# Performance work log

Hardware: AMD Instinct MI355X
Metric: run time of the kernel (lower is better)

The kernel has to match this reference:

```python
import jax, jax.numpy as jnp
import numpy as np

EPS = 1e-6  # torch nn.PairwiseDistance default eps


def setup_inputs() -> dict:
    key = jax.random.key(0)
    k1, k2 = jax.random.split(key)
    B, D, H, W = 4096, 512, 128, 128
    x = jax.random.normal(k1, (B, D), dtype=jnp.float32)
    weight = jax.random.normal(k2, (D, H * W), dtype=jnp.float32)  # SOM codebook (D, K)
    xs, ys = jnp.meshgrid(jnp.arange(H), jnp.arange(W), indexing="ij")
    locations = jnp.stack([xs.ravel(), ys.ravel()], axis=-1).astype(jnp.float32)  # (K, 2)
    return {"x": x, "weight": weight, "locations": locations}


def reference(x, weight, locations):
    # Faithful to torch: dists[b,k] = ||x[b,:] - weight[:,k] + eps||_2 reduced over D,
    # then min over codes, gather BMU grid locations, mean min-distance loss.
    B, D = x.shape
    x2 = jnp.sum(x * x, axis=1, keepdims=True)            # (B,1)
    w2 = jnp.sum(weight * weight, axis=0, keepdims=True)  # (1,K)
    cross = x @ weight                                     # (B,K) GEMM
    # exact expansion of sum_d (x - w + eps)^2
    lin = 2.0 * EPS * (jnp.sum(x, axis=1, keepdims=True) - jnp.sum(weight, axis=0, keepdims=True))
    d2 = x2 - 2.0 * cross + w2 + lin + jnp.float32(D) * EPS * EPS  # (B,K)
    dists = jnp.sqrt(jnp.maximum(d2, 0.0))
    losses = jnp.min(dists, axis=1, keepdims=True)         # (B,1)
    bmu_idx = jnp.argmin(dists, axis=1)                    # (B,)
    bmu_locations = locations[bmu_idx][:, None, :]         # (B,1,2) like locations[bmu_indexes]
    loss = jnp.sum(losses) / jnp.float32(B)
    return bmu_locations, loss
```

## Files before the change

### kernel.cpp

```cpp
#include <hip/hip_runtime.h>
#include <stdint.h>

#define B_ROWS 4096
#define D_DIM  512
#define K_CODES 16384
#define EPS 1e-6f

typedef __attribute__((ext_vector_type(8))) short short8;
typedef __attribute__((ext_vector_type(4))) float floatx4;

__device__ __forceinline__ unsigned short f2bf(float f) {
  unsigned int u = __float_as_uint(f);
  u += 0x7FFFu + ((u >> 16) & 1u);
  return (unsigned short)(u >> 16);
}
__device__ __forceinline__ float bf2f(unsigned short h) {
  return __uint_as_float(((unsigned int)h) << 16);
}

__device__ __forceinline__ void load_lds16(const short* g, short* l) {
  __builtin_amdgcn_global_load_lds(
      (const __attribute__((address_space(1))) void*)g,
      (__attribute__((address_space(3))) void*)l, 16, 0, 0);
}

__global__ void prep_kernel(const float* __restrict__ x,
                            const float* __restrict__ w,
                            short* __restrict__ A, short* __restrict__ W,
                            float* __restrict__ row_term,
                            float* __restrict__ colpart,
                            float* __restrict__ loss_acc,
                            unsigned int* __restrict__ counter) {
  const int bid = blockIdx.x;
  const int t = threadIdx.x;
  if (bid < 2048) {
    __shared__ float tile[64][65];
    const int k0 = (bid & 255) * 64;
    const int dchunk = bid >> 8;
    const int d0 = dchunk * 64;
#pragma unroll
    for (int i = 0; i < 4; ++i) {
      int idx = i * 256 + t;
      int r = idx >> 4, c4 = (idx & 15) * 4;
      float4 v = *(const float4*)&w[(size_t)(d0 + r) * K_CODES + k0 + c4];
      tile[r][c4 + 0] = v.x;
      tile[r][c4 + 1] = v.y;
      tile[r][c4 + 2] = v.z;
      tile[r][c4 + 3] = v.w;
    }
    __syncthreads();
    const int sub = t & 7;
    const int cd8 = sub * 8;
#pragma unroll
    for (int g = 0; g < 2; ++g) {
      const int rk = (t >> 3) + g * 32;
      short8 hi, lo;
      float s = 0.f, q = 0.f;
#pragma unroll
      for (int j = 0; j < 8; ++j) {
        float v = tile[cd8 + j][rk];
        s += v;
        q += v * v;
        unsigned short h = f2bf(v);
        float r2 = v - bf2f(h);
        hi[j] = (short)h;
        lo[j] = (short)f2bf(r2);
      }
      *(short8*)(W + (size_t)(k0 + rk) * 1024 + d0 + cd8) = hi;
      *(short8*)(W + (size_t)(k0 + rk) * 1024 + 512 + d0 + cd8) = lo;
#pragma unroll
      for (int m = 1; m < 8; m <<= 1) {
        s += __shfl_xor(s, m, 64);
        q += __shfl_xor(q, m, 64);
      }
      if (sub == 0)
        colpart[(size_t)dchunk * K_CODES + k0 + rk] = q - 2.0f * EPS * s;
    }
  } else {
    const int xb = bid - 2048;
    if (xb == 0 && t == 0) { loss_acc[0] = 0.0f; counter[0] = 0u; }
    const int wv = t >> 6, lane = t & 63;
#pragma unroll
    for (int i = 0; i < 4; ++i) {
      const int b = xb * 16 + i * 4 + wv;
      const float* xr = x + (size_t)b * D_DIM;
      float4 v0 = ((const float4*)xr)[lane * 2];
      float4 v1 = ((const float4*)xr)[lane * 2 + 1];
      float vals[8] = {v0.x, v0.y, v0.z, v0.w, v1.x, v1.y, v1.z, v1.w};
      short8 hi, lo;
      float s = 0.f, q = 0.f;
#pragma unroll
      for (int j = 0; j < 8; ++j) {
        float v = vals[j];
        s += v;
        q += v * v;
        unsigned short h = f2bf(v);
        float r = v - bf2f(h);
        hi[j] = (short)h;
        lo[j] = (short)f2bf(r);
      }
      *(short8*)(A + (size_t)b * 1024 + lane * 8) = hi;
      *(short8*)(A + (size_t)b * 1024 + 512 + lane * 8) = lo;
#pragma unroll
      for (int m = 1; m < 64; m <<= 1) {
        s += __shfl_xor(s, m, 64);
        q += __shfl_xor(q, m, 64);
      }
      if (lane == 0) row_term[b] = q + 2.0f * EPS * s + (float)D_DIM * EPS * EPS;
    }
  }
}

__global__ __launch_bounds__(256, 4) void som_gemm_kernel(
    const short* __restrict__ A, const short* __restrict__ W,
    const float* __restrict__ row_term, const float* __restrict__ colpart,
    unsigned long long* __restrict__ partial) {
  __shared__ __align__(16) short As[128 * 64];
  __shared__ __align__(16) short Bs[128 * 64];

  const int nt = blockIdx.x;
  const int mt = blockIdx.y;
  const int m0 = mt * 128, n0 = nt * 128;
  const int tid = threadIdx.x;
  const int wv = tid >> 6, lane = tid & 63;
  const int m_off = (wv & 1) * 64, n_off = (wv >> 1) * 64;
  const int q = lane >> 4, l15 = lane & 15;

  floatx4 acc[4][4];
  const floatx4 zero = {0.f, 0.f, 0.f, 0.f};
#pragma unroll
  for (int mi = 0; mi < 4; ++mi)
#pragma unroll
    for (int ni = 0; ni < 4; ++ni) acc[mi][ni] = zero;

  const int srow = lane >> 3;
  const int scol = ((lane & 7) ^ (srow & 7)) * 8;

  for (int kt = 0; kt < 24; ++kt) {
    const int a_k0 = (kt * 64) & 1023;
    const int w_k0 = (kt < 16) ? ((kt * 64) & 511) : (kt * 64 - 512);
    __syncthreads();
#pragma unroll
    for (int i = 0; i < 4; ++i) {
      const int c = wv * 4 + i;
      const int row = c * 8 + srow;
      load_lds16(A + (size_t)(m0 + row) * 1024 + a_k0 + scol, As + c * 512);
      load_lds16(W + (size_t)(n0 + row) * 1024 + w_k0 + scol, Bs + c * 512);
    }
    __syncthreads();
#pragma unroll
    for (int ks = 0; ks < 2; ++ks) {
      const int sw = ((ks * 4 + q) ^ (l15 & 7)) * 8;
      short8 af[4], bf[4];
#pragma unroll
      for (int mi = 0; mi < 4; ++mi)
        af[mi] = *(const short8*)(As + (m_off + mi * 16 + l15) * 64 + sw);
#pragma unroll
      for (int ni = 0; ni < 4; ++ni)
        bf[ni] = *(const short8*)(Bs + (n_off + ni * 16 + l15) * 64 + sw);
#pragma unroll
      for (int mi = 0; mi < 4; ++mi)
#pragma unroll
        for (int ni = 0; ni < 4; ++ni)
          acc[mi][ni] = __builtin_amdgcn_mfma_f32_16x16x32_bf16(
              af[mi], bf[ni], acc[mi][ni], 0, 0, 0);
    }
  }

  float ct[4];
#pragma unroll
  for (int ni = 0; ni < 4; ++ni) {
    const int k = n0 + n_off + ni * 16 + l15;
    float s = 0.f;
#pragma unroll
    for (int c = 0; c < 8; ++c) s += colpart[(size_t)c * K_CODES + k];
    ct[ni] = s;
  }
  float rt[16];
#pragma unroll
  for (int mi = 0; mi < 4; ++mi)
#pragma unroll
    for (int r = 0; r < 4; ++r)
      rt[mi * 4 + r] = row_term[m0 + m_off + mi * 16 + q * 4 + r];

  __syncthreads();
  unsigned long long* lds_min = (unsigned long long*)As;

#pragma unroll
  for (int mi = 0; mi < 4; ++mi) {
#pragma unroll
    for (int r = 0; r < 4; ++r) {
      unsigned long long v = ~0ull;
#pragma unroll
      for (int ni = 0; ni < 4; ++ni) {
        float d2 = rt[mi * 4 + r] + ct[ni] - 2.0f * acc[mi][ni][r];
        d2 = fmaxf(d2, 0.0f);
        unsigned long long p =
            ((unsigned long long)__float_as_uint(d2) << 32) |
            (unsigned int)(n0 + n_off + ni * 16 + l15);
        v = p < v ? p : v;
      }
#pragma unroll
      for (int mms = 1; mms < 16; mms <<= 1) {
        unsigned long long o = __shfl_xor(v, mms, 64);
        v = o < v ? o : v;
      }
      if (l15 == 0) lds_min[(wv >> 1) * 128 + m_off + mi * 16 + q * 4 + r] = v;
    }
  }
  __syncthreads();
  if (tid < 128) {
    unsigned long long v0 = lds_min[tid];
    unsigned long long v1 = lds_min[128 + tid];
    partial[(size_t)nt * B_ROWS + m0 + tid] = v1 < v0 ? v1 : v0;
  }
}

__global__ void finalize_kernel(const unsigned long long* __restrict__ partial,
                                const float* __restrict__ loc,
                                float* __restrict__ out,
                                float* __restrict__ loss_acc,
                                unsigned int* __restrict__ counter) {
  __shared__ unsigned long long red[4][64];
  const int t = threadIdx.x;
  const int rl = t & 63;
  const int p = t >> 6;
  const int b = blockIdx.x * 64 + rl;
  unsigned long long v = ~0ull;
#pragma unroll
  for (int i = 0; i < 32; ++i) {
    int nt = p * 32 + i;
    unsigned long long pv = partial[(size_t)nt * B_ROWS + b];
    v = pv < v ? pv : v;
  }
  red[p][rl] = v;
  __syncthreads();
  if (t < 64) {
    unsigned long long v0 = red[0][t], v1 = red[1][t];
    unsigned long long v2 = red[2][t], v3 = red[3][t];
    v0 = v1 < v0 ? v1 : v0;
    v2 = v3 < v2 ? v3 : v2;
    v0 = v2 < v0 ? v2 : v0;
    unsigned int k = (unsigned int)(v0 & 0xFFFFFFFFu);
    float d2 = __uint_as_float((unsigned int)(v0 >> 32));
    float dist = sqrtf(d2);
    int row = blockIdx.x * 64 + t;
    out[2 * row] = loc[2 * k];
    out[2 * row + 1] = loc[2 * k + 1];
    float s = dist;
#pragma unroll
    for (int m = 1; m < 64; m <<= 1) s += __shfl_xor(s, m, 64);
    if (t == 0) {
      atomicAdd(loss_acc, s);
      __threadfence();
      unsigned int old = atomicAdd(counter, 1u);
      if (old == gridDim.x - 1) {
        __threadfence();
        float total = atomicAdd(loss_acc, 0.0f);
        out[2 * B_ROWS] = total * (1.0f / (float)B_ROWS);
      }
    }
  }
}

extern "C" void kernel_launch(void* const* d_in, const int* in_sizes, int n_in,
                              void* d_out, int out_size, void* d_ws, size_t ws_size,
                              hipStream_t stream) {
  const float* x = (const float*)d_in[0];
  const float* w = (const float*)d_in[1];
  const float* loc = (const float*)d_in[2];
  float* out = (float*)d_out;
  char* ws = (char*)d_ws;

  short* A = (short*)(ws + 0);
  short* W = (short*)(ws + 8388608);
  float* row_term = (float*)(ws + 41943040);
  float* colpart = (float*)(ws + 41959424);
  unsigned long long* partial = (unsigned long long*)(ws + 42483712);
  float* loss_acc = (float*)(ws + 46678016);
  unsigned int* counter = (unsigned int*)(ws + 46678020);

  prep_kernel<<<2304, 256, 0, stream>>>(x, w, A, W, row_term, colpart,
                                        loss_acc, counter);
  som_gemm_kernel<<<dim3(K_CODES / 128, B_ROWS / 128), 256, 0, stream>>>(
      A, W, row_term, colpart, partial);
  finalize_kernel<<<B_ROWS / 64, 256, 0, stream>>>(partial, loc, out, loss_acc,
                                                   counter);
}
```

Baseline: 288.9 us.

## Add dedicated producer wave with double-buffered LDS to overlap loads and MFMA

The GEMM block grows to five waves. The extra wave does all global-to-LDS loads for the next K-tile into a second LDS buffer while the four compute waves run MFMAs on the current buffer. This removes one barrier per K step and aims to hide global load latency behind compute. In exchange, LDS per block doubles and the launch bounds drop to two blocks per CU. A single wave now has to issue every load, which could make load issue the bottleneck.

```diff
diff --git a/kernel.cpp b/kernel.cpp
--- a/kernel.cpp
+++ b/kernel.cpp
@@ -111,12 +111,12 @@
   }
 }
 
-__global__ __launch_bounds__(256, 4) void som_gemm_kernel(
+__global__ __launch_bounds__(320, 2) void som_gemm_kernel(
     const short* __restrict__ A, const short* __restrict__ W,
     const float* __restrict__ row_term, const float* __restrict__ colpart,
     unsigned long long* __restrict__ partial) {
-  __shared__ __align__(16) short As[128 * 64];
-  __shared__ __align__(16) short Bs[128 * 64];
+  __shared__ __align__(16) short As[2][128 * 64];
+  __shared__ __align__(16) short Bs[2][128 * 64];
 
   const int nt = blockIdx.x;
   const int mt = blockIdx.y;
@@ -126,6 +126,9 @@
   const int m_off = (wv & 1) * 64, n_off = (wv >> 1) * 64;
   const int q = lane >> 4, l15 = lane & 15;
 
+  const int srow = lane >> 3;
+  const int scol = ((lane & 7) ^ (srow & 7)) * 8;
+
   floatx4 acc[4][4];
   const floatx4 zero = {0.f, 0.f, 0.f, 0.f};
 #pragma unroll
@@ -133,79 +136,97 @@
 #pragma unroll
     for (int ni = 0; ni < 4; ++ni) acc[mi][ni] = zero;
 
-  const int srow = lane >> 3;
-  const int scol = ((lane & 7) ^ (srow & 7)) * 8;
+  if (wv == 4) {
+#pragma unroll
+    for (int c = 0; c < 16; ++c) {
+      load_lds16(A + (size_t)(m0 + c * 8 + srow) * 1024 + scol, As[0] + c * 512);
+      load_lds16(W + (size_t)(n0 + c * 8 + srow) * 1024 + scol, Bs[0] + c * 512);
+    }
+  }
 
   for (int kt = 0; kt < 24; ++kt) {
-    const int a_k0 = (kt * 64) & 1023;
-    const int w_k0 = (kt < 16) ? ((kt * 64) & 511) : (kt * 64 - 512);
     __syncthreads();
-#pragma unroll
-    for (int i = 0; i < 4; ++i) {
-      const int c = wv * 4 + i;
-      const int row = c * 8 + srow;
-      load_lds16(A + (size_t)(m0 + row) * 1024 + a_k0 + scol, As + c * 512);
-      load_lds16(W + (size_t)(n0 + row) * 1024 + w_k0 + scol, Bs + c * 512);
-    }
-    __syncthreads();
-#pragma unroll
-    for (int ks = 0; ks < 2; ++ks) {
-      const int sw = ((ks * 4 + q) ^ (l15 & 7)) * 8;
-      short8 af[4], bf[4];
-#pragma unroll
-      for (int mi = 0; mi < 4; ++mi)
-        af[mi] = *(const short8*)(As + (m_off + mi * 16 + l15) * 64 + sw);
-#pragma unroll
-      for (int ni = 0; ni < 4; ++ni)
-        bf[ni] = *(const short8*)(Bs + (n_off + ni * 16 + l15) * 64 + sw);
-#pragma unroll
-      for (int mi = 0; mi < 4; ++mi)
+    if (wv == 4) {
+      if (kt < 23) {
+        const int kn = kt + 1;
+        const int a_k0 = (kn * 64) & 1023;
+        const int w_k0 = (kn < 16) ? ((kn * 64) & 511) : (kn * 64 - 512);
+        short* as = As[kn & 1];
+        short* bs = Bs[kn & 1];
+#pragma unroll
+        for (int c = 0; c < 16; ++c) {
+          load_lds16(A + (size_t)(m0 + c * 8 + srow) * 1024 + a_k0 + scol,
+                     as + c * 512);
+          load_lds16(W + (size_t)(n0 + c * 8 + srow) * 1024 + w_k0 + scol,
+                     bs + c * 512);
+        }
+      }
+    } else {
+      const short* as = As[kt & 1];
+      const short* bs = Bs[kt & 1];
+#pragma unroll
+      for (int ks = 0; ks < 2; ++ks) {
+        const int sw = ((ks * 4 + q) ^ (l15 & 7)) * 8;
+        short8 af[4], bf[4];
+#pragma unroll
+        for (int mi = 0; mi < 4; ++mi)
+          af[mi] = *(const short8*)(as + (m_off + mi * 16 + l15) * 64 + sw);
 #pragma unroll
         for (int ni = 0; ni < 4; ++ni)
-          acc[mi][ni] = __builtin_amdgcn_mfma_f32_16x16x32_bf16(
-              af[mi], bf[ni], acc[mi][ni], 0, 0, 0);
+          bf[ni] = *(const short8*)(bs + (n_off + ni * 16 + l15) * 64 + sw);
+#pragma unroll
+        for (int mi = 0; mi < 4; ++mi)
+#pragma unroll
+          for (int ni = 0; ni < 4; ++ni)
+            acc[mi][ni] = __builtin_amdgcn_mfma_f32_16x16x32_bf16(
+                af[mi], bf[ni], acc[mi][ni], 0, 0, 0);
+      }
     }
   }
 
   float ct[4];
-#pragma unroll
-  for (int ni = 0; ni < 4; ++ni) {
-    const int k = n0 + n_off + ni * 16 + l15;
-    float s = 0.f;
-#pragma unroll
-    for (int c = 0; c < 8; ++c) s += colpart[(size_t)c * K_CODES + k];
-    ct[ni] = s;
-  }
   float rt[16];
-#pragma unroll
-  for (int mi = 0; mi < 4; ++mi)
-#pragma unroll
-    for (int r = 0; r < 4; ++r)
-      rt[mi * 4 + r] = row_term[m0 + m_off + mi * 16 + q * 4 + r];
+  if (wv < 4) {
+#pragma unroll
+    for (int ni = 0; ni < 4; ++ni) {
+      const int k = n0 + n_off + ni * 16 + l15;
+      float s = 0.f;
+#pragma unroll
+      for (int c = 0; c < 8; ++c) s += colpart[(size_t)c * K_CODES + k];
+      ct[ni] = s;
+    }
+#pragma unroll
+    for (int mi = 0; mi < 4; ++mi)
+#pragma unroll
+      for (int r = 0; r < 4; ++r)
+        rt[mi * 4 + r] = row_term[m0 + m_off + mi * 16 + q * 4 + r];
+  }
 
   __syncthreads();
-  unsigned long long* lds_min = (unsigned long long*)As;
-
-#pragma unroll
-  for (int mi = 0; mi < 4; ++mi) {
-#pragma unroll
-    for (int r = 0; r < 4; ++r) {
-      unsigned long long v = ~0ull;
-#pragma unroll
-      for (int ni = 0; ni < 4; ++ni) {
-        float d2 = rt[mi * 4 + r] + ct[ni] - 2.0f * acc[mi][ni][r];
-        d2 = fmaxf(d2, 0.0f);
-        unsigned long long p =
-            ((unsigned long long)__float_as_uint(d2) << 32) |
-            (unsigned int)(n0 + n_off + ni * 16 + l15);
-        v = p < v ? p : v;
-      }
-#pragma unroll
-      for (int mms = 1; mms < 16; mms <<= 1) {
-        unsigned long long o = __shfl_xor(v, mms, 64);
-        v = o < v ? o : v;
-      }
-      if (l15 == 0) lds_min[(wv >> 1) * 128 + m_off + mi * 16 + q * 4 + r] = v;
+  unsigned long long* lds_min = (unsigned long long*)&As[0][0];
+
+  if (wv < 4) {
+#pragma unroll
+    for (int mi = 0; mi < 4; ++mi) {
+#pragma unroll
+      for (int r = 0; r < 4; ++r) {
+        unsigned long long v = ~0ull;
+#pragma unroll
+        for (int ni = 0; ni < 4; ++ni) {
+          float d2 = rt[mi * 4 + r] + ct[ni] - 2.0f * acc[mi][ni][r];
+          d2 = fmaxf(d2, 0.0f);
+          unsigned long long p =
+              ((unsigned long long)__float_as_uint(d2) << 32) |
+              (unsigned int)(n0 + n_off + ni * 16 + l15);
+          v = p < v ? p : v;
+        }
+#pragma unroll
+        for (int mms = 1; mms < 16; mms <<= 1) {
+          unsigned long long o = __shfl_xor(v, mms, 64);
+          v = o < v ? o : v;
+        }
+        if (l15 == 0) lds_min[(wv >> 1) * 128 + m_off + mi * 16 + q * 4 + r] = v;
+      }
     }
   }
   __syncthreads();
@@ -282,7 +303,7 @@
 
   prep_kernel<<<2304, 256, 0, stream>>>(x, w, A, W, row_term, colpart,
                                         loss_acc, counter);
-  som_gemm_kernel<<<dim3(K_CODES / 128, B_ROWS / 128), 256, 0, stream>>>(
+  som_gemm_kernel<<<dim3(K_CODES / 128, B_ROWS / 128), 320, 0, stream>>>(
       A, W, row_term, colpart, partial);
   finalize_kernel<<<B_ROWS / 64, 256, 0, stream>>>(partial, loc, out, loss_acc,
                                                    counter);
```

After: 483.0 us. 1.67x slower.

## Fuse finalize into GEMM via last-block-per-row-tile reduction; widen prep tiles

Applied to the files above, without the earlier changes.

Removes the separate finalize kernel. Each GEMM block now bumps a per-row-tile atomic counter, and the last block to finish a row tile reduces the 128 column partials, writes the BMU locations and adds to the loss. A second counter picks the block that writes the mean loss. Separately, the prep kernel's weight-transpose blocks now cover 128 codes each instead of 64, halving the block count. This saves one kernel launch and the tail of a separate pass, at the cost of fences and a serial tail reduction inside the last GEMM blocks.

```diff
diff --git a/kernel.cpp b/kernel.cpp
--- a/kernel.cpp
+++ b/kernel.cpp
@@ -30,29 +30,30 @@
                             float* __restrict__ row_term,
                             float* __restrict__ colpart,
                             float* __restrict__ loss_acc,
-                            unsigned int* __restrict__ counter) {
+                            unsigned int* __restrict__ counter2,
+                            unsigned int* __restrict__ cnt) {
   const int bid = blockIdx.x;
   const int t = threadIdx.x;
-  if (bid < 2048) {
-    __shared__ float tile[64][65];
-    const int k0 = (bid & 255) * 64;
-    const int dchunk = bid >> 8;
+  if (bid < 1024) {
+    __shared__ float tile[64][129];
+    const int k0 = (bid & 127) * 128;
+    const int dchunk = bid >> 7;
     const int d0 = dchunk * 64;
 #pragma unroll
-    for (int i = 0; i < 4; ++i) {
+    for (int i = 0; i < 8; ++i) {
       int idx = i * 256 + t;
-      int r = idx >> 4, c4 = (idx & 15) * 4;
-      float4 v = *(const float4*)&w[(size_t)(d0 + r) * K_CODES + k0 + c4];
-      tile[r][c4 + 0] = v.x;
-      tile[r][c4 + 1] = v.y;
-      tile[r][c4 + 2] = v.z;
-      tile[r][c4 + 3] = v.w;
+      int r = idx >> 5, c = (idx & 31) * 4;
+      float4 v = *(const float4*)&w[(size_t)(d0 + r) * K_CODES + k0 + c];
+      tile[r][c + 0] = v.x;
+      tile[r][c + 1] = v.y;
+      tile[r][c + 2] = v.z;
+      tile[r][c + 3] = v.w;
     }
     __syncthreads();
     const int sub = t & 7;
     const int cd8 = sub * 8;
 #pragma unroll
-    for (int g = 0; g < 2; ++g) {
+    for (int g = 0; g < 4; ++g) {
       const int rk = (t >> 3) + g * 32;
       short8 hi, lo;
       float s = 0.f, q = 0.f;
@@ -77,8 +78,11 @@
         colpart[(size_t)dchunk * K_CODES + k0 + rk] = q - 2.0f * EPS * s;
     }
   } else {
-    const int xb = bid - 2048;
-    if (xb == 0 && t == 0) { loss_acc[0] = 0.0f; counter[0] = 0u; }
+    const int xb = bid - 1024;
+    if (xb == 0) {
+      if (t == 0) { loss_acc[0] = 0.0f; counter2[0] = 0u; }
+      if (t < 32) cnt[t] = 0u;
+    }
     const int wv = t >> 6, lane = t & 63;
 #pragma unroll
     for (int i = 0; i < 4; ++i) {
@@ -114,9 +118,13 @@
 __global__ __launch_bounds__(256, 4) void som_gemm_kernel(
     const short* __restrict__ A, const short* __restrict__ W,
     const float* __restrict__ row_term, const float* __restrict__ colpart,
-    unsigned long long* __restrict__ partial) {
+    unsigned long long* __restrict__ partial,
+    const float* __restrict__ loc, float* __restrict__ out,
+    float* __restrict__ loss_acc, unsigned int* __restrict__ counter2,
+    unsigned int* __restrict__ cnt) {
   __shared__ __align__(16) short As[128 * 64];
   __shared__ __align__(16) short Bs[128 * 64];
+  __shared__ int flag_s;
 
   const int nt = blockIdx.x;
   const int mt = blockIdx.y;
@@ -214,47 +222,49 @@
     unsigned long long v1 = lds_min[128 + tid];
     partial[(size_t)nt * B_ROWS + m0 + tid] = v1 < v0 ? v1 : v0;
   }
-}
-
-__global__ void finalize_kernel(const unsigned long long* __restrict__ partial,
-                                const float* __restrict__ loc,
-                                float* __restrict__ out,
-                                float* __restrict__ loss_acc,
-                                unsigned int* __restrict__ counter) {
-  __shared__ unsigned long long red[4][64];
-  const int t = threadIdx.x;
-  const int rl = t & 63;
-  const int p = t >> 6;
-  const int b = blockIdx.x * 64 + rl;
-  unsigned long long v = ~0ull;
-#pragma unroll
-  for (int i = 0; i < 32; ++i) {
-    int nt = p * 32 + i;
-    unsigned long long pv = partial[(size_t)nt * B_ROWS + b];
-    v = pv < v ? pv : v;
-  }
-  red[p][rl] = v;
-  __syncthreads();
-  if (t < 64) {
-    unsigned long long v0 = red[0][t], v1 = red[1][t];
-    unsigned long long v2 = red[2][t], v3 = red[3][t];
-    v0 = v1 < v0 ? v1 : v0;
-    v2 = v3 < v2 ? v3 : v2;
-    v0 = v2 < v0 ? v2 : v0;
-    unsigned int k = (unsigned int)(v0 & 0xFFFFFFFFu);
-    float d2 = __uint_as_float((unsigned int)(v0 >> 32));
-    float dist = sqrtf(d2);
-    int row = blockIdx.x * 64 + t;
-    out[2 * row] = loc[2 * k];
-    out[2 * row + 1] = loc[2 * k + 1];
-    float s = dist;
-#pragma unroll
-    for (int m = 1; m < 64; m <<= 1) s += __shfl_xor(s, m, 64);
-    if (t == 0) {
-      atomicAdd(loss_acc, s);
+
+  __threadfence();
+  __syncthreads();
+  if (tid == 0) {
+    unsigned int old = atomicAdd(&cnt[mt], 1u);
+    flag_s = (old == 127u) ? 1 : 0;
+  }
+  __syncthreads();
+  if (flag_s) {
+    __threadfence();
+    const int row = tid & 127;
+    const int half = tid >> 7;
+    unsigned long long v = ~0ull;
+#pragma unroll 8
+    for (int i = 0; i < 64; ++i) {
+      const int ntt = half * 64 + i;
+      unsigned long long p = partial[(size_t)ntt * B_ROWS + m0 + row];
+      v = p < v ? p : v;
+    }
+    unsigned long long* red = (unsigned long long*)As;
+    red[tid] = v;
+    __syncthreads();
+    float* wsum = (float*)Bs;
+    if (tid < 128) {
+      unsigned long long a = red[tid], b = red[tid + 128];
+      a = b < a ? b : a;
+      unsigned int k = (unsigned int)(a & 0xFFFFFFFFu);
+      float d2 = __uint_as_float((unsigned int)(a >> 32));
+      float dist = sqrtf(d2);
+      const int rg = m0 + tid;
+      out[2 * rg] = loc[2 * k];
+      out[2 * rg + 1] = loc[2 * k + 1];
+      float s = dist;
+#pragma unroll
+      for (int m = 1; m < 64; m <<= 1) s += __shfl_xor(s, m, 64);
+      if ((tid & 63) == 0) wsum[tid >> 6] = s;
+    }
+    __syncthreads();
+    if (tid == 0) {
+      atomicAdd(loss_acc, wsum[0] + wsum[1]);
       __threadfence();
-      unsigned int old = atomicAdd(counter, 1u);
-      if (old == gridDim.x - 1) {
+      unsigned int o2 = atomicAdd(counter2, 1u);
+      if (o2 == 31u) {
         __threadfence();
         float total = atomicAdd(loss_acc, 0.0f);
         out[2 * B_ROWS] = total * (1.0f / (float)B_ROWS);
@@ -278,12 +288,11 @@
   float* colpart = (float*)(ws + 41959424);
   unsigned long long* partial = (unsigned long long*)(ws + 42483712);
   float* loss_acc = (float*)(ws + 46678016);
-  unsigned int* counter = (unsigned int*)(ws + 46678020);
-
-  prep_kernel<<<2304, 256, 0, stream>>>(x, w, A, W, row_term, colpart,
-                                        loss_acc, counter);
+  unsigned int* counter2 = (unsigned int*)(ws + 46678020);
+  unsigned int* cnt = (unsigned int*)(ws + 46678024);
+
+  prep_kernel<<<1280, 256, 0, stream>>>(x, w, A, W, row_term, colpart,
+                                        loss_acc, counter2, cnt);
   som_gemm_kernel<<<dim3(K_CODES / 128, B_ROWS / 128), 256, 0, stream>>>(
-      A, W, row_term, colpart, partial);
-  finalize_kernel<<<B_ROWS / 64, 256, 0, stream>>>(partial, loc, out, loss_acc,
-                                                   counter);
-}
+      A, W, row_term, colpart, partial, loc, out, loss_acc, counter2, cnt);
+}
```

Result: slower. 663.2 us (+129.5%).
